# Kernel optimization log

Hardware: AMD Instinct MI355X
Metric: run time of the kernel (lower is better)

## Reference

```python
import jax, jax.numpy as jnp
import numpy as np

HIDDEN = 2304
HEADS = 16
THETA = 10000.0
LN_EPS = 1e-5


def setup_inputs() -> dict:
    key = jax.random.key(0)
    ks = jax.random.split(key, 6)
    d = HIDDEN
    init = lambda k, shape: jax.random.normal(k, shape, jnp.float32) * 0.02
    return {
        "x": jax.random.normal(ks[0], (4, 2048, d), jnp.float32),
        "wq": init(ks[1], (d, d)), "bq": jnp.zeros((d,), jnp.float32),
        "wk": init(ks[2], (d, d)), "bk": jnp.zeros((d,), jnp.float32),
        "wv": init(ks[3], (d, d)), "bv": jnp.zeros((d,), jnp.float32),
        "wo": init(ks[4], (d, d)), "bo": jnp.zeros((d,), jnp.float32),
        "ln_g": jnp.ones((d,), jnp.float32),
        "ln_b": jnp.zeros((d,), jnp.float32),
    }


def reference(x, wq, bq, wk, bk, wv, bv, wo, bo, ln_g, ln_b):
    b, s, d = x.shape
    H = HEADS
    Dh = d // H

    # qkv projections (nn.Linear: x @ W^T + b)
    q = jnp.einsum('bsd,ed->bse', x, wq) + bq
    k = jnp.einsum('bsd,ed->bse', x, wk) + bk
    v = jnp.einsum('bsd,ed->bse', x, wv) + bv

    # RoPE over the FULL hidden dim (d/2 pairs), as in the source
    pos = jnp.arange(s, dtype=jnp.float32)                    # (s,)
    scale = jnp.arange(0, d, 2, dtype=jnp.float32) / d        # (d/2,)
    omega = 1.0 / (THETA ** scale)                            # (d/2,)
    ang = pos[:, None] * omega[None, :]                       # (s, d/2)
    cos, sin = jnp.cos(ang), jnp.sin(ang)

    def rot(t):
        t2 = t.reshape(b, s, d // 2, 2)
        x0, x1 = t2[..., 0], t2[..., 1]
        return jnp.stack([cos * x0 - sin * x1, sin * x0 + cos * x1], axis=-1).reshape(b, s, d)

    q, k = rot(q), rot(k)

    # split heads -> (b, H, s, Dh)
    q = q.reshape(b, s, H, Dh).transpose(0, 2, 1, 3)
    k = k.reshape(b, s, H, Dh).transpose(0, 2, 1, 3)
    v = v.reshape(b, s, H, Dh).transpose(0, 2, 1, 3)

    # NOTE: faithful to source: einsum labels make this HEAD-mixing
    # attention at each position: logits shape (b, H, s, H)
    att_scale = 1.0 / (Dh ** 0.5)
    logits = jnp.einsum('bnhd,bmhd->bnhm', q, k) * att_scale
    w = jax.nn.softmax(logits, axis=-1)                       # (b,H,s,H)
    out = jnp.einsum('bnhm,bmhd->bnhd', w, v)                 # (b,H,s,Dh)

    out = out.transpose(0, 2, 1, 3).reshape(b, s, d)
    out = jnp.einsum('bsd,ed->bse', out, wo) + bo

    # residual + LayerNorm (dropout in eval mode -> identity)
    y = x + out
    mu = jnp.mean(y, axis=-1, keepdims=True)
    var = jnp.mean((y - mu) ** 2, axis=-1, keepdims=True)
    return (y - mu) * jax.lax.rsqrt(var + LN_EPS) * ln_g + ln_b
```

## Files before the change

kernel.cpp:

```cpp
#include <hip/hip_runtime.h>
#include <stdint.h>
#include <stddef.h>

#define D_HID 2304
#define NTOK  8192
#define NQKV  6912
#define WELEMS 5308416
#define SEQ_MASK 2047

typedef unsigned short u16;
typedef __bf16 bf16x8 __attribute__((ext_vector_type(8)));
typedef float  f32x16 __attribute__((ext_vector_type(16)));
typedef float  f32x4  __attribute__((ext_vector_type(4)));

__device__ __forceinline__ u16 f2bf(float f) {
    unsigned int u = __builtin_bit_cast(unsigned int, f);
    u += 0x7fffu + ((u >> 16) & 1u);
    return (u16)(u >> 16);
}
__device__ __forceinline__ float bf2f(u16 h) {
    unsigned int u = ((unsigned int)h) << 16;
    return __builtin_bit_cast(float, u);
}

__device__ __forceinline__ void gl2lds16(const void* g, void* l) {
    __builtin_amdgcn_global_load_lds(
        (const __attribute__((address_space(1))) void*)g,
        (__attribute__((address_space(3))) void*)l,
        16, 0, 0);
}

__global__ __launch_bounds__(256) void cvt_f32_bf16(
    const float* __restrict__ src, u16* __restrict__ dst)
{
    size_t i = ((size_t)blockIdx.x * 256 + threadIdx.x) * 4;
    float4 f = *(const float4*)(src + i);
    ushort4 o = make_ushort4(f2bf(f.x), f2bf(f.y), f2bf(f.z), f2bf(f.w));
    *(ushort4*)(dst + i) = o;
}

__global__ __launch_bounds__(256) void cvt_weights(
    const float* __restrict__ wq, const float* __restrict__ wk,
    const float* __restrict__ wv, const float* __restrict__ wo,
    u16* __restrict__ dst,
    const float* __restrict__ bq, const float* __restrict__ bk,
    const float* __restrict__ bv, float* __restrict__ bqkv)
{
    int i = blockIdx.x * 256 + threadIdx.x;
    if (i < NQKV)
        bqkv[i] = (i < 2304) ? bq[i] : (i < 4608) ? bk[i - 2304] : bv[i - 4608];
    size_t base = (size_t)i * 4;
    int r = (int)(base / WELEMS);
    const float* src = (r == 0) ? wq : (r == 1) ? wk : (r == 2) ? wv : wo;
    float4 f = *(const float4*)(src + (base - (size_t)r * WELEMS));
    ushort4 o = make_ushort4(f2bf(f.x), f2bf(f.y), f2bf(f.z), f2bf(f.w));
    *(ushort4*)(dst + base) = o;
}

__global__ __launch_bounds__(512, 2) void gemm256_bt(
    const u16* __restrict__ A, const u16* __restrict__ B,
    const float* __restrict__ bias, u16* __restrict__ Cout,
    int M, int N, int K)
{
    __shared__ __align__(16) u16 lds2[65536];

    const int tid  = threadIdx.x;
    const int lane = tid & 63;
    const int wave = tid >> 6;
    const int NT   = K >> 6;
    (void)M;

    const int chunk = gridDim.x >> 3;
    const int bid = (blockIdx.x & 7) * chunk + (blockIdx.x >> 3);
    const int num_bn = N >> 8;
    const int bm = bid / num_bn;
    const int bn = bid - bm * num_bn;

    const int srow = lane >> 3;
    const u16* __restrict__ Ast = A + (size_t)(bm * 256 + wave * 8 + srow) * K
                                    + ((lane & 7) ^ srow) * 8;
    const u16* __restrict__ Bst = B + (size_t)(bn * 256 + wave * 8 + srow) * K
                                    + ((lane & 7) ^ srow) * 8;
    const size_t row64  = (size_t)64 * K;
    const size_t row128 = (size_t)128 * K;
    const int ldsW = wave * 512;

#define STAGE(buf, hsel, tt) do {                                              \
    const u16* g_ = ((hsel) < 2 ? Ast : Bst)                                   \
                    + (((hsel) & 1) ? row128 : 0) + (size_t)(tt) * 64;         \
    u16* l_ = lds2 + (buf) * 32768 + (((hsel) < 2) ? 0 : 16384)                \
              + (((hsel) & 1) ? 8192 : 0) + ldsW;                              \
    gl2lds16(g_, l_);                                                          \
    gl2lds16(g_ + row64, l_ + 4096);                                           \
} while (0)

    const int l15 = lane & 15, l4 = lane >> 4;
    const int aBase = (wave >> 2) * 8192 + l15 * 64;
    const int bBase = 16384 + ((wave >> 1) & 1) * 8192
                      + ((wave & 1) * 64 + l15) * 64;
    const int s0 = ((l4    ) ^ (lane & 7)) * 8;
    const int s1 = ((l4 + 4) ^ (lane & 7)) * 8;

    f32x4 acc[8][4] = {};

    STAGE(0, 2, 0); STAGE(0, 3, 0); STAGE(0, 0, 0); STAGE(0, 1, 0);
    STAGE(1, 2, 1); STAGE(1, 3, 1); STAGE(1, 0, 1);
    asm volatile("s_waitcnt vmcnt(6)" ::: "memory");
    __builtin_amdgcn_s_barrier();

    for (int t = 0; t < NT; ++t) {
        const int cur = t & 1;
        const u16* lc = lds2 + cur * 32768;
        const bool stg2 = (t + 2 < NT);
        bf16x8 bfr[4][2], am[2][2], ah[4][2];

#pragma unroll
        for (int n = 0; n < 4; ++n) {
            bfr[n][0] = *(const bf16x8*)(lc + bBase + n * 1024 + s0);
            bfr[n][1] = *(const bf16x8*)(lc + bBase + n * 1024 + s1);
        }
#pragma unroll
        for (int mo = 0; mo < 2; ++mo) {
            am[mo][0] = *(const bf16x8*)(lc + aBase + mo * 1024 + s0);
            am[mo][1] = *(const bf16x8*)(lc + aBase + mo * 1024 + s1);
        }
        if (t + 1 < NT) STAGE(cur ^ 1, 1, t + 1);
        __builtin_amdgcn_s_barrier();
        asm volatile("s_waitcnt lgkmcnt(0)" ::: "memory");
        __builtin_amdgcn_sched_barrier(0);
        __builtin_amdgcn_s_setprio(1);
#pragma unroll
        for (int kk = 0; kk < 2; ++kk)
#pragma unroll
            for (int mo = 0; mo < 2; ++mo)
#pragma unroll
                for (int n = 0; n < 4; ++n)
                    acc[mo][n] = __builtin_amdgcn_mfma_f32_16x16x32_bf16(
                        am[mo][kk], bfr[n][kk], acc[mo][n], 0, 0, 0);
        __builtin_amdgcn_s_setprio(0);
        __builtin_amdgcn_s_barrier();

#pragma unroll
        for (int mo = 0; mo < 2; ++mo) {
            am[mo][0] = *(const bf16x8*)(lc + aBase + (2 + mo) * 1024 + s0);
            am[mo][1] = *(const bf16x8*)(lc + aBase + (2 + mo) * 1024 + s1);
        }
        if (stg2) STAGE(cur, 2, t + 2);
        __builtin_amdgcn_s_barrier();
        asm volatile("s_waitcnt lgkmcnt(0)" ::: "memory");
        __builtin_amdgcn_sched_barrier(0);
        __builtin_amdgcn_s_setprio(1);
#pragma unroll
        for (int kk = 0; kk < 2; ++kk)
#pragma unroll
            for (int mo = 0; mo < 2; ++mo)
#pragma unroll
                for (int n = 0; n < 4; ++n)
                    acc[2 + mo][n] = __builtin_amdgcn_mfma_f32_16x16x32_bf16(
                        am[mo][kk], bfr[n][kk], acc[2 + mo][n], 0, 0, 0);
        __builtin_amdgcn_s_setprio(0);
        __builtin_amdgcn_s_barrier();

#pragma unroll
        for (int mo = 0; mo < 4; ++mo) {
            ah[mo][0] = *(const bf16x8*)(lc + aBase + (4 + mo) * 1024 + s0);
            ah[mo][1] = *(const bf16x8*)(lc + aBase + (4 + mo) * 1024 + s1);
        }
        if (stg2) STAGE(cur, 3, t + 2);
        __builtin_amdgcn_s_barrier();
        asm volatile("s_waitcnt lgkmcnt(0)" ::: "memory");
        __builtin_amdgcn_sched_barrier(0);
        __builtin_amdgcn_s_setprio(1);
#pragma unroll
        for (int kk = 0; kk < 2; ++kk)
#pragma unroll
            for (int mo = 0; mo < 2; ++mo)
#pragma unroll
                for (int n = 0; n < 4; ++n)
                    acc[4 + mo][n] = __builtin_amdgcn_mfma_f32_16x16x32_bf16(
                        ah[mo][kk], bfr[n][kk], acc[4 + mo][n], 0, 0, 0);
        __builtin_amdgcn_s_setprio(0);
        __builtin_amdgcn_s_barrier();

        if (stg2) STAGE(cur, 0, t + 2);
        __builtin_amdgcn_s_barrier();
        __builtin_amdgcn_s_setprio(1);
#pragma unroll
        for (int kk = 0; kk < 2; ++kk)
#pragma unroll
            for (int mo = 0; mo < 2; ++mo)
#pragma unroll
                for (int n = 0; n < 4; ++n)
                    acc[6 + mo][n] = __builtin_amdgcn_mfma_f32_16x16x32_bf16(
                        ah[2 + mo][kk], bfr[n][kk], acc[6 + mo][n], 0, 0, 0);
        __builtin_amdgcn_s_setprio(0);
        if (t < NT - 2)       asm volatile("s_waitcnt vmcnt(6)" ::: "memory");
        else if (t == NT - 2) asm volatile("s_waitcnt vmcnt(0)" ::: "memory");
        __builtin_amdgcn_s_barrier();
    }
#undef STAGE

    const int wm0 = (wave >> 2) * 128, wn0 = (wave & 3) * 64;
#pragma unroll
    for (int n = 0; n < 4; ++n) {
        const int gn = bn * 256 + wn0 + n * 16 + l15;
        const float bv = bias[gn];
#pragma unroll
        for (int m = 0; m < 8; ++m) {
            const int gm = bm * 256 + wm0 + m * 16 + l4 * 4;
#pragma unroll
            for (int j = 0; j < 4; ++j)
                Cout[(size_t)(gm + j) * N + gn] = f2bf(acc[m][n][j] + bv);
        }
    }
}

template<int MODE>
__global__ __launch_bounds__(256, 3) void gemm_bt(
    const u16* __restrict__ A, const u16* __restrict__ B,
    const float* __restrict__ bias, u16* __restrict__ Cout,
    const u16* __restrict__ resid, int M, int N, int K)
{
    __shared__ __align__(16) u16 As[128 * 64];
    __shared__ __align__(16) u16 Bs[128 * 64];

    const int tid  = threadIdx.x;
    const int lane = tid & 63;
    const int wave = tid >> 6;

    const int num_bn = N >> 7;
    const int rem = blockIdx.x % (num_bn << 3);
    const int bn  = rem >> 3;
    const int bm  = ((blockIdx.x / (num_bn << 3)) << 3) + (rem & 7);

    const int srow = tid >> 3;
    const int sc   = (tid & 7) ^ (srow & 7);
    const u16* Ag = A + (size_t)(bm * 128 + srow) * K + sc * 8;
    const u16* Bg = B + (size_t)(bn * 128 + srow) * K + sc * 8;
    const size_t row32 = (size_t)32 * K;
    u16* asd = As + wave * 512;
    u16* bsd = Bs + wave * 512;

    const int rl = lane & 31;
    const int h  = lane >> 5;
    const int swz = rl & 7;
    const int wm = (wave >> 1) * 64;
    const int wn = (wave & 1) * 64;

    f32x16 acc[2][2] = {};

    for (int kb = 0; kb < K; kb += 64) {
        __syncthreads();
#pragma unroll
        for (int r = 0; r < 4; ++r) {
            gl2lds16(Ag + kb + r * row32, asd + r * 2048);
            gl2lds16(Bg + kb + r * row32, bsd + r * 2048);
        }
        __syncthreads();

#pragma unroll
        for (int s = 0; s < 4; ++s) {
            const int ch = ((s * 2 + h) ^ swz) * 8;
            bf16x8 a0 = *(const bf16x8*)(As + (wm      + rl) * 64 + ch);
            bf16x8 a1 = *(const bf16x8*)(As + (wm + 32 + rl) * 64 + ch);
            bf16x8 b0 = *(const bf16x8*)(Bs + (wn      + rl) * 64 + ch);
            bf16x8 b1 = *(const bf16x8*)(Bs + (wn + 32 + rl) * 64 + ch);
            acc[0][0] = __builtin_amdgcn_mfma_f32_32x32x16_bf16(a0, b0, acc[0][0], 0, 0, 0);
            acc[0][1] = __builtin_amdgcn_mfma_f32_32x32x16_bf16(a0, b1, acc[0][1], 0, 0, 0);
            acc[1][0] = __builtin_amdgcn_mfma_f32_32x32x16_bf16(a1, b0, acc[1][0], 0, 0, 0);
            acc[1][1] = __builtin_amdgcn_mfma_f32_32x32x16_bf16(a1, b1, acc[1][1], 0, 0, 0);
        }
    }

#pragma unroll
    for (int mt = 0; mt < 2; ++mt) {
#pragma unroll
        for (int nt = 0; nt < 2; ++nt) {
            const int gn = bn * 128 + wn + nt * 32 + rl;
            const float bv = bias[gn];
#pragma unroll
            for (int reg = 0; reg < 16; ++reg) {
                const int gm = bm * 128 + wm + mt * 32 +
                               (reg & 3) + 8 * (reg >> 2) + 4 * h;
                const size_t idx = (size_t)gm * N + gn;
                float v = acc[mt][nt][reg] + bv;
                if constexpr (MODE == 1) v += bf2f(resid[idx]);
                Cout[idx] = f2bf(v);
            }
        }
    }
}

#define HROW 148
__global__ __launch_bounds__(256) void attn_headmix(
    const u16* __restrict__ QKV, u16* __restrict__ Aout)
{
    __shared__ __align__(16) float qs[16 * HROW];
    __shared__ __align__(16) float ks[16 * HROW];
    __shared__ __align__(16) float vs[16 * HROW];
    __shared__ __align__(16) float wsmT[256];

    const int tid = threadIdx.x;
    const int t   = blockIdx.x;
    const float fpos = (float)(t & SEQ_MASK);
    const u16* row = QKV + (size_t)t * NQKV;

    const float OMEGA_C = -2.0f * 13.287712379549449f / 2304.0f;
    const float INV2PI  = 0.15915494309189535f;

    for (int c = tid; c < 864; c += 256) {
        uint4 raw = *(const uint4*)(row + c * 8);
        float f[8];
        f[0] = bf2f(raw.x & 0xffff); f[1] = bf2f(raw.x >> 16);
        f[2] = bf2f(raw.y & 0xffff); f[3] = bf2f(raw.y >> 16);
        f[4] = bf2f(raw.z & 0xffff); f[5] = bf2f(raw.z >> 16);
        f[6] = bf2f(raw.w & 0xffff); f[7] = bf2f(raw.w >> 16);
        if (c < 576) {
            const int cc = (c < 288) ? c : c - 288;
            const int p0 = cc * 4;
#pragma unroll
            for (int jp = 0; jp < 4; ++jp) {
                float omega = exp2f((float)(p0 + jp) * OMEGA_C);
                float rr = fpos * omega * INV2PI;
                rr -= floorf(rr);
                float sn = __builtin_amdgcn_sinf(rr);
                float cs = __builtin_amdgcn_cosf(rr);
                float x0 = f[2 * jp], x1 = f[2 * jp + 1];
                f[2 * jp]     = cs * x0 - sn * x1;
                f[2 * jp + 1] = sn * x0 + cs * x1;
            }
            const int hr = cc / 18, col = (cc - hr * 18) * 8;
            float* dst = ((c < 288) ? qs : ks) + hr * HROW + col;
            *(float4*)(dst)     = make_float4(f[0], f[1], f[2], f[3]);
            *(float4*)(dst + 4) = make_float4(f[4], f[5], f[6], f[7]);
        } else {
            const int cv = c - 576;
            const int hr = cv / 18, col = (cv - hr * 18) * 8;
            float* dst = vs + hr * HROW + col;
            *(float4*)(dst)     = make_float4(f[0], f[1], f[2], f[3]);
            *(float4*)(dst + 4) = make_float4(f[4], f[5], f[6], f[7]);
        }
    }
    __syncthreads();

    const int n = tid >> 4, m = tid & 15;
    const float* qr = qs + n * HROW;
    const float* kr = ks + m * HROW;
    float s = 0.f;
#pragma unroll
    for (int d = 0; d < 144; d += 4) {
        float4 qv = *(const float4*)(qr + d);
        float4 kv = *(const float4*)(kr + d);
        s += qv.x * kv.x + qv.y * kv.y + qv.z * kv.z + qv.w * kv.w;
    }
    s *= (1.0f / 12.0f);

    float mx = s;
#pragma unroll
    for (int off = 8; off >= 1; off >>= 1) mx = fmaxf(mx, __shfl_xor(mx, off));
    float e = __expf(s - mx);
    float sum = e;
#pragma unroll
    for (int off = 8; off >= 1; off >>= 1) sum += __shfl_xor(sum, off);
    wsmT[m * 16 + n] = e / sum;
    __syncthreads();

    if (tid < 144) {
        const int col4 = tid % 36;
        const int nq   = tid / 36;
        const int oc   = col4 * 4;
        float4 a0 = {0,0,0,0}, a1 = {0,0,0,0}, a2 = {0,0,0,0}, a3 = {0,0,0,0};
#pragma unroll
        for (int mm = 0; mm < 16; ++mm) {
            float4 w4 = *(const float4*)(wsmT + mm * 16 + nq * 4);
            float4 v4 = *(const float4*)(vs + mm * HROW + oc);
            a0.x += w4.x * v4.x; a0.y += w4.x * v4.y; a0.z += w4.x * v4.z; a0.w += w4.x * v4.w;
            a1.x += w4.y * v4.x; a1.y += w4.y * v4.y; a1.z += w4.y * v4.z; a1.w += w4.y * v4.w;
            a2.x += w4.z * v4.x; a2.y += w4.z * v4.y; a2.z += w4.z * v4.z; a2.w += w4.z * v4.w;
            a3.x += w4.w * v4.x; a3.y += w4.w * v4.y; a3.z += w4.w * v4.z; a3.w += w4.w * v4.w;
        }
        u16* orow = Aout + (size_t)t * D_HID;
        float4 accs[4] = {a0, a1, a2, a3};
#pragma unroll
        for (int i = 0; i < 4; ++i) {
            const int nn = nq * 4 + i;
            ushort4 o = make_ushort4(f2bf(accs[i].x), f2bf(accs[i].y),
                                     f2bf(accs[i].z), f2bf(accs[i].w));
            *(ushort4*)(orow + nn * 144 + oc) = o;
        }
    }
}

__global__ __launch_bounds__(256) void ln_kernel(
    const u16* __restrict__ Y, const float* __restrict__ g,
    const float* __restrict__ b, float* __restrict__ out)
{
    const int tid  = threadIdx.x;
    const u16* y = Y + (size_t)blockIdx.x * D_HID;
    float v[9];
    float s = 0.f, s2 = 0.f;
#pragma unroll
    for (int r = 0; r < 9; ++r) {
        v[r] = bf2f(y[tid + r * 256]);
        s += v[r]; s2 += v[r] * v[r];
    }
#pragma unroll
    for (int off = 32; off >= 1; off >>= 1) {
        s  += __shfl_xor(s, off);
        s2 += __shfl_xor(s2, off);
    }
    __shared__ float red[8];
    const int wave = tid >> 6;
    if ((tid & 63) == 0) { red[wave] = s; red[4 + wave] = s2; }
    __syncthreads();
    s  = red[0] + red[1] + red[2] + red[3];
    s2 = red[4] + red[5] + red[6] + red[7];
    const float inv_n = 1.0f / 2304.0f;
    float mu  = s * inv_n;
    float var = fmaxf(s2 * inv_n - mu * mu, 0.f);
    float inv = rsqrtf(var + 1e-5f);
    float* orow = out + (size_t)blockIdx.x * D_HID;
#pragma unroll
    for (int r = 0; r < 9; ++r) {
        int c = tid + r * 256;
        orow[c] = (v[r] - mu) * inv * g[c] + b[c];
    }
}

extern "C" void kernel_launch(void* const* d_in, const int* in_sizes, int n_in,
                              void* d_out, int out_size, void* d_ws, size_t ws_size,
                              hipStream_t stream)
{
    const float* x   = (const float*)d_in[0];
    const float* wq  = (const float*)d_in[1];
    const float* bq  = (const float*)d_in[2];
    const float* wk  = (const float*)d_in[3];
    const float* bk  = (const float*)d_in[4];
    const float* wv  = (const float*)d_in[5];
    const float* bv  = (const float*)d_in[6];
    const float* wo  = (const float*)d_in[7];
    const float* bo  = (const float*)d_in[8];
    const float* lng = (const float*)d_in[9];
    const float* lnb = (const float*)d_in[10];

    char* ws = (char*)d_ws;
    size_t off = 0;
    auto alloc = [&](size_t bytes) {
        void* p = ws + off;
        off += (bytes + 255) & ~(size_t)255;
        return p;
    };
    u16*   xb   = (u16*)alloc((size_t)NTOK * D_HID * 2);
    u16*   wqkv = (u16*)alloc((size_t)(NQKV + D_HID) * D_HID * 2);
    u16*   wob  = wqkv + (size_t)NQKV * D_HID;
    float* bqkv = (float*)alloc((size_t)NQKV * 4);
    u16*   qkv  = (u16*)alloc((size_t)NTOK * NQKV * 2);
    u16*   aout = (u16*)alloc((size_t)NTOK * D_HID * 2);
    u16*   ybuf = qkv;

    cvt_f32_bf16<<<NTOK * D_HID / 1024, 256, 0, stream>>>(x, xb);
    cvt_weights<<<4 * WELEMS / 1024, 256, 0, stream>>>(wq, wk, wv, wo, wqkv,
                                                       bq, bk, bv, bqkv);
    gemm256_bt<<<(NTOK / 256) * (NQKV / 256), 512, 0, stream>>>(
        xb, wqkv, bqkv, qkv, NTOK, NQKV, D_HID);
    attn_headmix<<<NTOK, 256, 0, stream>>>(qkv, aout);
    gemm_bt<1><<<(D_HID / 128) * (NTOK / 128), 256, 0, stream>>>(
        aout, wob, bo, ybuf, xb, NTOK, D_HID, D_HID);
    ln_kernel<<<NTOK, 256, 0, stream>>>(ybuf, lng, lnb, (float*)d_out);
}
```

Baseline: 660.8 us.

## Software-pipeline LDS fragment loads across K-halves in GEMM main loop

Restructures the GEMM inner loop so operand fragments are split by K-half (s0/s1), and loads for the next phase, including the next tile's first K-half, are issued before the current MFMA block. The goal is to hide LDS read latency behind MFMA work instead of waiting on lgkmcnt right before each compute block. It also reorders the global-to-LDS staging waits and barriers. In exchange it holds more live fragment registers and relies on a more intricate barrier and vmcnt ordering that could race if miscounted.

```diff
diff --git a/kernel.cpp b/kernel.cpp
--- a/kernel.cpp
+++ b/kernel.cpp
@@ -102,100 +102,104 @@
     const int s1 = ((l4 + 4) ^ (lane & 7)) * 8;
 
     f32x4 acc[8][4] = {};
+    bf16x8 Bk0[4], Bk1[4], Aev[4], Aod[4];
 
     STAGE(0, 2, 0); STAGE(0, 3, 0); STAGE(0, 0, 0); STAGE(0, 1, 0);
     STAGE(1, 2, 1); STAGE(1, 3, 1); STAGE(1, 0, 1);
     asm volatile("s_waitcnt vmcnt(6)" ::: "memory");
     __builtin_amdgcn_s_barrier();
+#pragma unroll
+    for (int n = 0; n < 4; ++n)
+        Bk0[n] = *(const bf16x8*)(lds2 + bBase + n * 1024 + s0);
+#pragma unroll
+    for (int mo = 0; mo < 4; ++mo)
+        Aev[mo] = *(const bf16x8*)(lds2 + aBase + mo * 1024 + s0);
 
     for (int t = 0; t < NT; ++t) {
         const int cur = t & 1;
         const u16* lc = lds2 + cur * 32768;
-        const bool stg2 = (t + 2 < NT);
-        bf16x8 bfr[4][2], am[2][2], ah[4][2];
-
-#pragma unroll
-        for (int n = 0; n < 4; ++n) {
-            bfr[n][0] = *(const bf16x8*)(lc + bBase + n * 1024 + s0);
-            bfr[n][1] = *(const bf16x8*)(lc + bBase + n * 1024 + s1);
-        }
-#pragma unroll
-        for (int mo = 0; mo < 2; ++mo) {
-            am[mo][0] = *(const bf16x8*)(lc + aBase + mo * 1024 + s0);
-            am[mo][1] = *(const bf16x8*)(lc + aBase + mo * 1024 + s1);
-        }
-        if (t + 1 < NT) STAGE(cur ^ 1, 1, t + 1);
+        const u16* ln = lds2 + (cur ^ 1) * 32768;
+        const bool st1 = (t + 1 < NT);
+        const bool st2 = (t + 2 < NT);
+
+#pragma unroll
+        for (int n = 0; n < 4; ++n)
+            Bk1[n] = *(const bf16x8*)(lc + bBase + n * 1024 + s1);
+#pragma unroll
+        for (int mo = 0; mo < 4; ++mo)
+            Aod[mo] = *(const bf16x8*)(lc + aBase + (4 + mo) * 1024 + s0);
+        if (st1) STAGE(cur ^ 1, 1, t + 1);
+        __builtin_amdgcn_sched_barrier(0);
+        __builtin_amdgcn_s_setprio(1);
+#pragma unroll
+        for (int mo = 0; mo < 4; ++mo)
+#pragma unroll
+            for (int n = 0; n < 4; ++n)
+                acc[mo][n] = __builtin_amdgcn_mfma_f32_16x16x32_bf16(
+                    Aev[mo], Bk0[n], acc[mo][n], 0, 0, 0);
+        __builtin_amdgcn_s_setprio(0);
+        __builtin_amdgcn_sched_barrier(0);
         __builtin_amdgcn_s_barrier();
+
+#pragma unroll
+        for (int mo = 0; mo < 4; ++mo)
+            Aev[mo] = *(const bf16x8*)(lc + aBase + mo * 1024 + s1);
+        if (st2) STAGE(cur, 2, t + 2);
+        __builtin_amdgcn_sched_barrier(0);
+        __builtin_amdgcn_s_setprio(1);
+#pragma unroll
+        for (int mo = 0; mo < 4; ++mo)
+#pragma unroll
+            for (int n = 0; n < 4; ++n)
+                acc[4 + mo][n] = __builtin_amdgcn_mfma_f32_16x16x32_bf16(
+                    Aod[mo], Bk0[n], acc[4 + mo][n], 0, 0, 0);
+        __builtin_amdgcn_s_setprio(0);
+        __builtin_amdgcn_sched_barrier(0);
         asm volatile("s_waitcnt lgkmcnt(0)" ::: "memory");
+        __builtin_amdgcn_s_barrier();
+
+#pragma unroll
+        for (int mo = 0; mo < 4; ++mo)
+            Aod[mo] = *(const bf16x8*)(lc + aBase + (4 + mo) * 1024 + s1);
+        if (st2) STAGE(cur, 3, t + 2);
+        if (st2)      asm volatile("s_waitcnt vmcnt(4)" ::: "memory");
+        else if (st1) asm volatile("s_waitcnt vmcnt(0)" ::: "memory");
+        if (st1) {
+            __builtin_amdgcn_s_barrier();
+#pragma unroll
+            for (int n = 0; n < 4; ++n)
+                Bk0[n] = *(const bf16x8*)(ln + bBase + n * 1024 + s0);
+        }
         __builtin_amdgcn_sched_barrier(0);
         __builtin_amdgcn_s_setprio(1);
 #pragma unroll
-        for (int kk = 0; kk < 2; ++kk)
-#pragma unroll
-            for (int mo = 0; mo < 2; ++mo)
-#pragma unroll
-                for (int n = 0; n < 4; ++n)
-                    acc[mo][n] = __builtin_amdgcn_mfma_f32_16x16x32_bf16(
-                        am[mo][kk], bfr[n][kk], acc[mo][n], 0, 0, 0);
+        for (int mo = 0; mo < 4; ++mo)
+#pragma unroll
+            for (int n = 0; n < 4; ++n)
+                acc[mo][n] = __builtin_amdgcn_mfma_f32_16x16x32_bf16(
+                    Aev[mo], Bk1[n], acc[mo][n], 0, 0, 0);
         __builtin_amdgcn_s_setprio(0);
+        __builtin_amdgcn_sched_barrier(0);
+        asm volatile("s_waitcnt lgkmcnt(0)" ::: "memory");
         __builtin_amdgcn_s_barrier();
 
-#pragma unroll
-        for (int mo = 0; mo < 2; ++mo) {
-            am[mo][0] = *(const bf16x8*)(lc + aBase + (2 + mo) * 1024 + s0);
-            am[mo][1] = *(const bf16x8*)(lc + aBase + (2 + mo) * 1024 + s1);
-        }
-        if (stg2) STAGE(cur, 2, t + 2);
-        __builtin_amdgcn_s_barrier();
+        if (st2) STAGE(cur, 0, t + 2);
+        if (st1) {
+#pragma unroll
+            for (int mo = 0; mo < 4; ++mo)
+                Aev[mo] = *(const bf16x8*)(ln + aBase + mo * 1024 + s0);
+        }
+        __builtin_amdgcn_sched_barrier(0);
+        __builtin_amdgcn_s_setprio(1);
+#pragma unroll
+        for (int mo = 0; mo < 4; ++mo)
+#pragma unroll
+            for (int n = 0; n < 4; ++n)
+                acc[4 + mo][n] = __builtin_amdgcn_mfma_f32_16x16x32_bf16(
+                    Aod[mo], Bk1[n], acc[4 + mo][n], 0, 0, 0);
+        __builtin_amdgcn_s_setprio(0);
+        __builtin_amdgcn_sched_barrier(0);
         asm volatile("s_waitcnt lgkmcnt(0)" ::: "memory");
-        __builtin_amdgcn_sched_barrier(0);
-        __builtin_amdgcn_s_setprio(1);
-#pragma unroll
-        for (int kk = 0; kk < 2; ++kk)
-#pragma unroll
-            for (int mo = 0; mo < 2; ++mo)
-#pragma unroll
-                for (int n = 0; n < 4; ++n)
-                    acc[2 + mo][n] = __builtin_amdgcn_mfma_f32_16x16x32_bf16(
-                        am[mo][kk], bfr[n][kk], acc[2 + mo][n], 0, 0, 0);
-        __builtin_amdgcn_s_setprio(0);
-        __builtin_amdgcn_s_barrier();
-
-#pragma unroll
-        for (int mo = 0; mo < 4; ++mo) {
-            ah[mo][0] = *(const bf16x8*)(lc + aBase + (4 + mo) * 1024 + s0);
-            ah[mo][1] = *(const bf16x8*)(lc + aBase + (4 + mo) * 1024 + s1);
-        }
-        if (stg2) STAGE(cur, 3, t + 2);
-        __builtin_amdgcn_s_barrier();
-        asm volatile("s_waitcnt lgkmcnt(0)" ::: "memory");
-        __builtin_amdgcn_sched_barrier(0);
-        __builtin_amdgcn_s_setprio(1);
-#pragma unroll
-        for (int kk = 0; kk < 2; ++kk)
-#pragma unroll
-            for (int mo = 0; mo < 2; ++mo)
-#pragma unroll
-                for (int n = 0; n < 4; ++n)
-                    acc[4 + mo][n] = __builtin_amdgcn_mfma_f32_16x16x32_bf16(
-                        ah[mo][kk], bfr[n][kk], acc[4 + mo][n], 0, 0, 0);
-        __builtin_amdgcn_s_setprio(0);
-        __builtin_amdgcn_s_barrier();
-
-        if (stg2) STAGE(cur, 0, t + 2);
-        __builtin_amdgcn_s_barrier();
-        __builtin_amdgcn_s_setprio(1);
-#pragma unroll
-        for (int kk = 0; kk < 2; ++kk)
-#pragma unroll
-            for (int mo = 0; mo < 2; ++mo)
-#pragma unroll
-                for (int n = 0; n < 4; ++n)
-                    acc[6 + mo][n] = __builtin_amdgcn_mfma_f32_16x16x32_bf16(
-                        ah[2 + mo][kk], bfr[n][kk], acc[6 + mo][n], 0, 0, 0);
-        __builtin_amdgcn_s_setprio(0);
-        if (t < NT - 2)       asm volatile("s_waitcnt vmcnt(6)" ::: "memory");
-        else if (t == NT - 2) asm volatile("s_waitcnt vmcnt(0)" ::: "memory");
         __builtin_amdgcn_s_barrier();
     }
 #undef STAGE
```

Measured after the change: 654.9 us. No clear change (-0.9%).
